# Optimization experiments

Measured on AMD Instinct MI355X. Metric: run time of the kernel, lower is better.

## Reference

```python
import jax, jax.numpy as jnp
import numpy as np

N = 8192
K = 64

def setup_inputs() -> dict:
    key = jax.random.key(0)
    kw, ky = jax.random.split(key)
    W = jax.random.uniform(kw, (N, N), dtype=jnp.float32)
    Y = jax.random.normal(ky, (N, K), dtype=jnp.float32)
    return {"W": W, "Y": Y}

def reference(W, Y):
    # SpectralNetLoss(normalized=False):
    #   Dy[i,j] = ||y_i - y_j||^2 ; loss = sum(W * Dy) / (2n)
    n = Y.shape[0]
    sq = jnp.sum(Y * Y, axis=1)                      # (n,)
    # squared pairwise distances: ||y_i||^2 + ||y_j||^2 - 2 y_i.y_j
    Dy = sq[:, None] + sq[None, :] - 2.0 * (Y @ Y.T)  # (n, n)
    Dy = jnp.maximum(Dy, 0.0)  # clamp tiny negatives from cancellation (cdist is nonneg)
    loss = jnp.sum(W * Dy) / (2.0 * n)
    return loss
```

## Files before the change

kernel.cpp:

```cpp
#include <hip/hip_runtime.h>
#include <stdint.h>

#define N 8192
#define K 64
#define JT_PER 8

typedef __attribute__((ext_vector_type(8))) short bf16x8;
typedef __attribute__((ext_vector_type(4))) float floatx4;
typedef __attribute__((ext_vector_type(4))) unsigned short ushort4v;

__global__ __launch_bounds__(256) void prep_kernel(const float* __restrict__ Y,
                                                   unsigned short* __restrict__ Ybf,
                                                   float* __restrict__ sq,
                                                   float* __restrict__ out) {
    if (blockIdx.x == 0 && threadIdx.x == 0) out[0] = 0.0f;
    const int t = blockIdx.x * 256 + threadIdx.x;
    floatx4 v = *reinterpret_cast<const floatx4*>(Y + (size_t)t * 4);
    ushort4v o;
    #pragma unroll
    for (int e = 0; e < 4; ++e) {
        uint32_t bits = __float_as_uint(v[e]);
        uint32_t rnd  = bits + 0x7FFF + ((bits >> 16) & 1);
        o[e] = (unsigned short)(rnd >> 16);
    }
    *reinterpret_cast<ushort4v*>(Ybf + (size_t)t * 4) = o;
    float s = v[0]*v[0] + v[1]*v[1] + v[2]*v[2] + v[3]*v[3];
    #pragma unroll
    for (int m = 8; m >= 1; m >>= 1) s += __shfl_xor(s, m, 64);
    if ((threadIdx.x & 15) == 0) sq[t >> 4] = s;
}

__global__ __launch_bounds__(256, 4) void loss_kernel(const float* __restrict__ W,
                                                      const unsigned short* __restrict__ Ybf,
                                                      const float* __restrict__ sq,
                                                      float* __restrict__ out) {
    __shared__ float wsum[4];

    const int bid  = blockIdx.x;
    const int i0   = (bid >> 5) * 128;
    const int j0   = (bid & 31) * 256;
    const int tid  = threadIdx.x;
    const int wv   = tid >> 6;
    const int lane = tid & 63;
    const int laneM = lane & 15;
    const int kq    = lane >> 4;
    const int iw    = i0 + wv * 32;

    bf16x8 a[2][2];
    float  sqi[2];
    #pragma unroll
    for (int mt = 0; mt < 2; ++mt) {
        const int row = iw + mt * 16 + laneM;
        a[mt][0] = *reinterpret_cast<const bf16x8*>(Ybf + (size_t)row * K + kq * 8);
        a[mt][1] = *reinterpret_cast<const bf16x8*>(Ybf + (size_t)row * K + 32 + kq * 8);
        sqi[mt]  = sq[row];
    }

    const float* wp0 = W + (size_t)(iw + laneM) * N + j0 + kq * 4;
    const float* wp1 = wp0 + (size_t)16 * N;

    floatx4 wbuf[2][2][2];
    #pragma unroll
    for (int nt = 0; nt < 2; ++nt) {
        wbuf[0][0][nt] = *reinterpret_cast<const floatx4*>(wp0 + nt * 16);
        wbuf[0][1][nt] = *reinterpret_cast<const floatx4*>(wp1 + nt * 16);
    }

    float p0 = 0.f, p1 = 0.f, p2 = 0.f, p3 = 0.f;

    #pragma unroll
    for (int jt = 0; jt < JT_PER; ++jt) {
        const int pp = jt & 1;
        const int jb = j0 + jt * 32;

        bf16x8  b[2][2];
        floatx4 sjq[2];
        #pragma unroll
        for (int nt = 0; nt < 2; ++nt) {
            const int rowj = jb + nt * 16 + laneM;
            b[nt][0] = *reinterpret_cast<const bf16x8*>(Ybf + (size_t)rowj * K + kq * 8);
            b[nt][1] = *reinterpret_cast<const bf16x8*>(Ybf + (size_t)rowj * K + 32 + kq * 8);
            sjq[nt]  = *reinterpret_cast<const floatx4*>(sq + jb + nt * 16 + kq * 4);
        }

        if (jt + 1 < JT_PER) {
            #pragma unroll
            for (int nt = 0; nt < 2; ++nt) {
                wbuf[pp ^ 1][0][nt] = *reinterpret_cast<const floatx4*>(wp0 + (jt + 1) * 32 + nt * 16);
                wbuf[pp ^ 1][1][nt] = *reinterpret_cast<const floatx4*>(wp1 + (jt + 1) * 32 + nt * 16);
            }
        }

        floatx4 acc[2][2];
        #pragma unroll
        for (int mt = 0; mt < 2; ++mt)
            #pragma unroll
            for (int nt = 0; nt < 2; ++nt) acc[mt][nt] = (floatx4){0.f, 0.f, 0.f, 0.f};
        #pragma unroll
        for (int ks = 0; ks < 2; ++ks)
            #pragma unroll
            for (int mt = 0; mt < 2; ++mt)
                #pragma unroll
                for (int nt = 0; nt < 2; ++nt)
                    acc[mt][nt] = __builtin_amdgcn_mfma_f32_16x16x32_bf16(b[nt][ks], a[mt][ks], acc[mt][nt], 0, 0, 0);

        #pragma unroll
        for (int mt = 0; mt < 2; ++mt) {
            const float si = sqi[mt];
            #pragma unroll
            for (int nt = 0; nt < 2; ++nt) {
                const floatx4 g  = acc[mt][nt];
                const floatx4 w4 = wbuf[pp][mt][nt];
                const floatx4 sj = sjq[nt];
                p0 = fmaf(w4[0], fmaxf(si + sj[0] - 2.0f * g[0], 0.f), p0);
                p1 = fmaf(w4[1], fmaxf(si + sj[1] - 2.0f * g[1], 0.f), p1);
                p2 = fmaf(w4[2], fmaxf(si + sj[2] - 2.0f * g[2], 0.f), p2);
                p3 = fmaf(w4[3], fmaxf(si + sj[3] - 2.0f * g[3], 0.f), p3);
            }
        }
    }

    float partial = (p0 + p1) + (p2 + p3);
    #pragma unroll
    for (int m = 32; m >= 1; m >>= 1) partial += __shfl_xor(partial, m, 64);
    if (lane == 0) wsum[wv] = partial;
    __syncthreads();
    if (tid == 0) {
        float tot = (wsum[0] + wsum[1]) + (wsum[2] + wsum[3]);
        atomicAdd(out, tot * (1.0f / (2.0f * (float)N)));
    }
}

extern "C" void kernel_launch(void* const* d_in, const int* in_sizes, int n_in,
                              void* d_out, int out_size, void* d_ws, size_t ws_size,
                              hipStream_t stream) {
    const float* W = (const float*)d_in[0];
    const float* Y = (const float*)d_in[1];
    float* out = (float*)d_out;

    unsigned short* Ybf = (unsigned short*)d_ws;
    float* sq = (float*)((char*)d_ws + (size_t)N * K * 2);

    prep_kernel<<<(N * K / 4) / 256, 256, 0, stream>>>(Y, Ybf, sq, out);
    loss_kernel<<<64 * 32, 256, 0, stream>>>(W, Ybf, sq, out);
}
```

Baseline: 365.3 us.

## Stage B tile and sq in LDS, deepen W prefetch to three stages

Each block now loads its 256-row slice of bf16 Y and the matching squared norms into shared memory once, cooperatively. Previously each of the four waves re-read them from global memory on every j-tile. The W register prefetch goes from double to triple buffering, issuing loads two tiles ahead so more HBM latency is hidden. This adds 32KB of LDS per block and more W registers, which may reduce occupancy under launch_bounds(256,4). It also adds a block-wide barrier before the main loop.

After: 362.6 us. About the same (-0.7%).

```diff
diff --git a/kernel.cpp b/kernel.cpp
--- a/kernel.cpp
+++ b/kernel.cpp
@@ -34,6 +34,8 @@
                                                       const unsigned short* __restrict__ Ybf,
                                                       const float* __restrict__ sq,
                                                       float* __restrict__ out) {
+    __shared__ __align__(16) bf16x8 lB[JT_PER * 2 * 2 * 64];
+    __shared__ __align__(16) float  lsq[256];
     __shared__ float wsum[4];
 
     const int bid  = blockIdx.x;
@@ -45,6 +47,20 @@
     const int laneM = lane & 15;
     const int kq    = lane >> 4;
     const int iw    = i0 + wv * 32;
+
+    #pragma unroll
+    for (int it = 0; it < 8; ++it) {
+        const int u  = it * 256 + tid;
+        const int l  = u & 63;
+        const int fb = u >> 6;
+        const int jt = fb >> 2;
+        const int nt = (fb >> 1) & 1;
+        const int ks = fb & 1;
+        lB[u] = *reinterpret_cast<const bf16x8*>(
+            Ybf + (size_t)(j0 + jt * 32 + nt * 16 + (l & 15)) * K + ks * 32 + (l >> 4) * 8);
+    }
+    if (tid < 64)
+        *reinterpret_cast<floatx4*>(&lsq[tid * 4]) = *reinterpret_cast<const floatx4*>(sq + j0 + tid * 4);
 
     bf16x8 a[2][2];
     float  sqi[2];
@@ -59,35 +75,38 @@
     const float* wp0 = W + (size_t)(iw + laneM) * N + j0 + kq * 4;
     const float* wp1 = wp0 + (size_t)16 * N;
 
-    floatx4 wbuf[2][2][2];
+    floatx4 wbuf[3][2][2];
     #pragma unroll
-    for (int nt = 0; nt < 2; ++nt) {
-        wbuf[0][0][nt] = *reinterpret_cast<const floatx4*>(wp0 + nt * 16);
-        wbuf[0][1][nt] = *reinterpret_cast<const floatx4*>(wp1 + nt * 16);
-    }
+    for (int g = 0; g < 2; ++g)
+        #pragma unroll
+        for (int nt = 0; nt < 2; ++nt) {
+            wbuf[g][0][nt] = *reinterpret_cast<const floatx4*>(wp0 + g * 32 + nt * 16);
+            wbuf[g][1][nt] = *reinterpret_cast<const floatx4*>(wp1 + g * 32 + nt * 16);
+        }
+
+    __syncthreads();
 
     float p0 = 0.f, p1 = 0.f, p2 = 0.f, p3 = 0.f;
 
     #pragma unroll
     for (int jt = 0; jt < JT_PER; ++jt) {
-        const int pp = jt & 1;
-        const int jb = j0 + jt * 32;
+        const int buf = jt % 3;
 
         bf16x8  b[2][2];
         floatx4 sjq[2];
         #pragma unroll
         for (int nt = 0; nt < 2; ++nt) {
-            const int rowj = jb + nt * 16 + laneM;
-            b[nt][0] = *reinterpret_cast<const bf16x8*>(Ybf + (size_t)rowj * K + kq * 8);
-            b[nt][1] = *reinterpret_cast<const bf16x8*>(Ybf + (size_t)rowj * K + 32 + kq * 8);
-            sjq[nt]  = *reinterpret_cast<const floatx4*>(sq + jb + nt * 16 + kq * 4);
+            b[nt][0] = lB[((jt * 2 + nt) * 2 + 0) * 64 + lane];
+            b[nt][1] = lB[((jt * 2 + nt) * 2 + 1) * 64 + lane];
+            sjq[nt]  = *reinterpret_cast<const floatx4*>(&lsq[jt * 32 + nt * 16 + kq * 4]);
         }
 
-        if (jt + 1 < JT_PER) {
+        if (jt + 2 < JT_PER) {
+            const int pb = (jt + 2) % 3;
             #pragma unroll
             for (int nt = 0; nt < 2; ++nt) {
-                wbuf[pp ^ 1][0][nt] = *reinterpret_cast<const floatx4*>(wp0 + (jt + 1) * 32 + nt * 16);
-                wbuf[pp ^ 1][1][nt] = *reinterpret_cast<const floatx4*>(wp1 + (jt + 1) * 32 + nt * 16);
+                wbuf[pb][0][nt] = *reinterpret_cast<const floatx4*>(wp0 + (jt + 2) * 32 + nt * 16);
+                wbuf[pb][1][nt] = *reinterpret_cast<const floatx4*>(wp1 + (jt + 2) * 32 + nt * 16);
             }
         }
 
@@ -110,7 +129,7 @@
             #pragma unroll
             for (int nt = 0; nt < 2; ++nt) {
                 const floatx4 g  = acc[mt][nt];
-                const floatx4 w4 = wbuf[pp][mt][nt];
+                const floatx4 w4 = wbuf[buf][mt][nt];
                 const floatx4 sj = sjq[nt];
                 p0 = fmaf(w4[0], fmaxf(si + sj[0] - 2.0f * g[0], 0.f), p0);
                 p1 = fmaf(w4[1], fmaxf(si + sj[1] - 2.0f * g[1], 0.f), p1);
```
